# Kernel tuning notes

Measured on AMD Instinct MI355X. Metric: run time of the kernel, lower is better.

The kernel has to match this reference:

```python
import jax, jax.numpy as jnp
import numpy as np

D_MODEL = 1024
N_HEADS = 16
D_K = D_MODEL // N_HEADS
EPS = 1e-5


def setup_inputs() -> dict:
    key = jax.random.key(0)
    ks = jax.random.split(key, 10)
    s = 1.0 / np.sqrt(D_MODEL)
    x = jax.random.normal(ks[0], (4, 2048, D_MODEL), dtype=jnp.float32)
    def lin(k):
        kw, kb = jax.random.split(k)
        W = jax.random.uniform(kw, (D_MODEL, D_MODEL), jnp.float32, -s, s)
        b = jax.random.uniform(kb, (D_MODEL,), jnp.float32, -s, s)
        return W, b
    Wq, bq = lin(ks[1])
    Wk, bk = lin(ks[2])
    Wv, bv = lin(ks[3])
    Wo, bo = lin(ks[4])
    gamma = jnp.ones((D_MODEL,), jnp.float32)
    beta = jnp.zeros((D_MODEL,), jnp.float32)
    return {"x": x, "Wq": Wq, "bq": bq, "Wk": Wk, "bk": bk,
            "Wv": Wv, "bv": bv, "Wo": Wo, "bo": bo,
            "gamma": gamma, "beta": beta}


def reference(x, Wq, bq, Wk, bk, Wv, bv, Wo, bo, gamma, beta):
    b, n, _ = x.shape
    residual = x
    # projections (PyTorch Linear: x @ W.T + b; here W stored as [in,out]-equivalent via transpose-free matmul)
    q = x @ Wq.T + bq
    k = x @ Wk.T + bk
    v = x @ Wv.T + bv
    # b n (h d) -> b h n d
    q = q.reshape(b, n, N_HEADS, D_K).transpose(0, 2, 1, 3)
    k = k.reshape(b, n, N_HEADS, D_K).transpose(0, 2, 1, 3)
    v = v.reshape(b, n, N_HEADS, D_K).transpose(0, 2, 1, 3)
    scores = jnp.einsum('bhnd,bhmd->bhnm', q, k) / jnp.sqrt(jnp.float32(D_K))
    attn = jax.nn.softmax(scores, axis=-1)
    out = jnp.einsum('bhnm,bhmd->bhnd', attn, v)
    out = out.transpose(0, 2, 1, 3).reshape(b, n, D_MODEL)
    out = out @ Wo.T + bo
    h = residual + out
    mu = jnp.mean(h, axis=-1, keepdims=True)
    var = jnp.var(h, axis=-1, keepdims=True)
    out_ln = (h - mu) / jnp.sqrt(var + EPS) * gamma + beta
    return (out_ln, attn)
```

## Files before the change

### kernel.cpp

```cpp
#include <hip/hip_runtime.h>
#include <math.h>

#define D_MODEL 1024
#define N_HEADS 16
#define D_K     64
#define SEQ     2048
#define BATCH   4
#define EPS     1e-5f
#define NT      (SEQ / 64)

typedef __attribute__((ext_vector_type(8))) short bf16x8;
typedef __attribute__((ext_vector_type(4))) float f32x4;

__device__ __forceinline__ unsigned short f2bf(float f) {
    unsigned u = __float_as_uint(f);
    u += 0x7fff + ((u >> 16) & 1);
    return (unsigned short)(u >> 16);
}

#define GLDS16(g, l) __builtin_amdgcn_global_load_lds( \
    (const __attribute__((address_space(1))) void*)(g), \
    (__attribute__((address_space(3))) void*)(l), 16, 0, 0)

__global__ __launch_bounds__(256) void cvt_f32_bf16(
    const float* __restrict__ in, unsigned short* __restrict__ out, int n4)
{
    int i = blockIdx.x * 256 + threadIdx.x;
    if (i >= n4) return;
    float4 f = ((const float4*)in)[i];
    union { ushort4 u; uint2 v; } o;
    o.u.x = f2bf(f.x); o.u.y = f2bf(f.y); o.u.z = f2bf(f.z); o.u.w = f2bf(f.w);
    ((uint2*)out)[i] = o.v;
}

__global__ __launch_bounds__(256) void gemm_qkv(
    const unsigned short* __restrict__ A,
    const unsigned short* __restrict__ Bq, const unsigned short* __restrict__ Bk,
    const unsigned short* __restrict__ Bv,
    const float* __restrict__ biq, const float* __restrict__ bik,
    const float* __restrict__ biv,
    unsigned short* __restrict__ Oq, unsigned short* __restrict__ Ok,
    unsigned short* __restrict__ Ov)
{
    const int which = blockIdx.x >> 3;
    const unsigned short* B = which == 0 ? Bq : (which == 1 ? Bk : Bv);
    const float* bias        = which == 0 ? biq : (which == 1 ? bik : biv);
    unsigned short* O        = which == 0 ? Oq : (which == 1 ? Ok : Ov);
    const float scale        = which == 0 ? 0.125f : 1.0f;

    __shared__ unsigned short As[128 * 32];
    __shared__ unsigned short Bs[128 * 32];
    const int tid = threadIdx.x;
    const int w = tid >> 6, lane = tid & 63;
    const int l15 = lane & 15, lh = lane >> 4;
    const int wm = w >> 1, wn = w & 1;
    const int bm = blockIdx.y * 128, bn = (blockIdx.x & 7) * 128;
    const int K = D_MODEL, N = D_MODEL;

    const int srow = lane >> 2;
    const int skk  = (lane & 3) * 8;

    f32x4 acc[4][4] = {};

    for (int k0 = 0; k0 < K; k0 += 32) {
#pragma unroll
        for (int cc = 0; cc < 2; ++cc) {
            int chunk = w * 2 + cc;
            int row = chunk * 16 + srow;
            GLDS16(A + (size_t)(bm + row) * K + k0 + skk, As + chunk * 512);
            GLDS16(B + (size_t)(bn + row) * K + k0 + skk, Bs + chunk * 512);
        }
        __syncthreads();
        bf16x8 af[4], bfr[4];
#pragma unroll
        for (int mi = 0; mi < 4; ++mi)
            af[mi] = *(const bf16x8*)&As[(wm * 64 + mi * 16 + l15) * 32 + lh * 8];
#pragma unroll
        for (int nj = 0; nj < 4; ++nj)
            bfr[nj] = *(const bf16x8*)&Bs[(wn * 64 + nj * 16 + l15) * 32 + lh * 8];
#pragma unroll
        for (int mi = 0; mi < 4; ++mi)
#pragma unroll
            for (int nj = 0; nj < 4; ++nj)
                acc[mi][nj] = __builtin_amdgcn_mfma_f32_16x16x32_bf16(
                    af[mi], bfr[nj], acc[mi][nj], 0, 0, 0);
        __syncthreads();
    }

#pragma unroll
    for (int mi = 0; mi < 4; ++mi) {
#pragma unroll
        for (int nj = 0; nj < 4; ++nj) {
            int col = bn + wn * 64 + nj * 16 + l15;
            float bv = bias[col];
#pragma unroll
            for (int r = 0; r < 4; ++r) {
                int row = bm + wm * 64 + mi * 16 + lh * 4 + r;
                O[(size_t)row * N + col] = f2bf((acc[mi][nj][r] + bv) * scale);
            }
        }
    }
}

__global__ __launch_bounds__(256) void gemm_out(
    const unsigned short* __restrict__ A, const unsigned short* __restrict__ B,
    const float* __restrict__ bias, const float* __restrict__ res,
    float* __restrict__ C)
{
    __shared__ unsigned short As[128 * 32];
    __shared__ unsigned short Bs[128 * 32];
    const int tid = threadIdx.x;
    const int w = tid >> 6, lane = tid & 63;
    const int l15 = lane & 15, lh = lane >> 4;
    const int wm = w >> 1, wn = w & 1;
    const int bm = blockIdx.y * 128, bn = blockIdx.x * 128;
    const int K = D_MODEL, N = D_MODEL;

    const int srow = lane >> 2;
    const int skk  = (lane & 3) * 8;

    f32x4 acc[4][4] = {};

    for (int k0 = 0; k0 < K; k0 += 32) {
#pragma unroll
        for (int cc = 0; cc < 2; ++cc) {
            int chunk = w * 2 + cc;
            int row = chunk * 16 + srow;
            GLDS16(A + (size_t)(bm + row) * K + k0 + skk, As + chunk * 512);
            GLDS16(B + (size_t)(bn + row) * K + k0 + skk, Bs + chunk * 512);
        }
        __syncthreads();
        bf16x8 af[4], bfr[4];
#pragma unroll
        for (int mi = 0; mi < 4; ++mi)
            af[mi] = *(const bf16x8*)&As[(wm * 64 + mi * 16 + l15) * 32 + lh * 8];
#pragma unroll
        for (int nj = 0; nj < 4; ++nj)
            bfr[nj] = *(const bf16x8*)&Bs[(wn * 64 + nj * 16 + l15) * 32 + lh * 8];
#pragma unroll
        for (int mi = 0; mi < 4; ++mi)
#pragma unroll
            for (int nj = 0; nj < 4; ++nj)
                acc[mi][nj] = __builtin_amdgcn_mfma_f32_16x16x32_bf16(
                    af[mi], bfr[nj], acc[mi][nj], 0, 0, 0);
        __syncthreads();
    }

#pragma unroll
    for (int mi = 0; mi < 4; ++mi) {
#pragma unroll
        for (int nj = 0; nj < 4; ++nj) {
            int col = bn + wn * 64 + nj * 16 + l15;
            float bv = bias[col];
#pragma unroll
            for (int r = 0; r < 4; ++r) {
                int row = bm + wm * 64 + mi * 16 + lh * 4 + r;
                C[(size_t)row * N + col] = acc[mi][nj][r] + bv + res[(size_t)row * N + col];
            }
        }
    }
}

__global__ __launch_bounds__(256) void transpose_v(
    const unsigned short* __restrict__ v, unsigned short* __restrict__ vt)
{
    __shared__ unsigned short T[64][72];
    const int bh = blockIdx.y, b = bh >> 4, h = bh & 15;
    const int s0 = blockIdx.x * 64;
    const int tid = threadIdx.x;
#pragma unroll
    for (int i = 0; i < 2; ++i) {
        int idx = i * 256 + tid;
        int sr = idx >> 3, dc = idx & 7;
        uint4 t = *(const uint4*)(v + ((size_t)b * SEQ + s0 + sr) * D_MODEL + h * 64 + dc * 8);
        *(uint4*)&T[sr][dc * 8] = t;
    }
    __syncthreads();
#pragma unroll
    for (int i = 0; i < 2; ++i) {
        int idx = i * 256 + tid;
        int d = idx >> 3, sc = idx & 7;
        unsigned short tmp[8];
#pragma unroll
        for (int j = 0; j < 8; ++j) tmp[j] = T[sc * 8 + j][d];
        *(uint4*)(vt + ((size_t)bh * 64 + d) * SEQ + s0 + sc * 8) = *(uint4*)tmp;
    }
}

__device__ __forceinline__ void stage_tile64(
    const unsigned short* __restrict__ gbase, size_t grow_stride,
    unsigned short* lds, int w, int lane)
{
#pragma unroll
    for (int i = 0; i < 2; ++i) {
        int row = i * 32 + w * 8 + (lane >> 3);
        int c   = (lane & 7) ^ (row & 7);
        GLDS16(gbase + (size_t)row * grow_stride + c * 8,
               lds + (size_t)(i * 256 + w * 64) * 8);
    }
}

__global__ __launch_bounds__(256) void attn_pass0(
    const unsigned short* __restrict__ qb, const unsigned short* __restrict__ kb,
    float* __restrict__ invl)
{
    __shared__ unsigned short Ks[2][64 * 64];
    const int bh = blockIdx.x, b = bh >> 4, head = bh & 15;
    const int tid = threadIdx.x;
    const int w = tid >> 6, lane = tid & 63, l15 = lane & 15, lh = lane >> 4;
    const int bq = blockIdx.y * 128 + w * 32;
    const size_t rowbase = (size_t)b * SEQ;
    const unsigned short* Kh = kb + rowbase * D_MODEL + head * 64;

    bf16x8 aq[2][2];
#pragma unroll
    for (int qs = 0; qs < 2; ++qs)
#pragma unroll
        for (int kd = 0; kd < 2; ++kd)
            aq[qs][kd] = *(const bf16x8*)(qb + (rowbase + bq + qs * 16 + l15) * D_MODEL
                                          + head * 64 + kd * 32 + lh * 8);

    float rsum[2] = {0.f, 0.f};

    stage_tile64(Kh, D_MODEL, Ks[0], w, lane);
    __syncthreads();

    for (int kt = 0; kt < NT; ++kt) {
        const int cur = kt & 1;
        if (kt + 1 < NT)
            stage_tile64(Kh + (size_t)(kt + 1) * 64 * D_MODEL, D_MODEL, Ks[cur ^ 1], w, lane);

        const char* kbuf = (const char*)Ks[cur];
        f32x4 s[2][4] = {};
#pragma unroll
        for (int fj = 0; fj < 4; ++fj) {
            int key = fj * 16 + l15;
            bf16x8 kf0 = *(const bf16x8*)(kbuf + key * 128 + ((lh ^ (key & 7)) << 4));
            bf16x8 kf1 = *(const bf16x8*)(kbuf + key * 128 + (((4 + lh) ^ (key & 7)) << 4));
#pragma unroll
            for (int qs = 0; qs < 2; ++qs) {
                s[qs][fj] = __builtin_amdgcn_mfma_f32_16x16x32_bf16(kf0, aq[qs][0], s[qs][fj], 0, 0, 0);
                s[qs][fj] = __builtin_amdgcn_mfma_f32_16x16x32_bf16(kf1, aq[qs][1], s[qs][fj], 0, 0, 0);
            }
        }
#pragma unroll
        for (int qs = 0; qs < 2; ++qs)
#pragma unroll
            for (int fj = 0; fj < 4; ++fj)
                rsum[qs] += (__expf(s[qs][fj][0]) + __expf(s[qs][fj][1]))
                          + (__expf(s[qs][fj][2]) + __expf(s[qs][fj][3]));
        __syncthreads();
    }

#pragma unroll
    for (int qs = 0; qs < 2; ++qs) {
        float v = rsum[qs];
        v += __shfl_xor(v, 16, 64);
        v += __shfl_xor(v, 32, 64);
        if (lh == 0)
            invl[(size_t)bh * SEQ + bq + qs * 16 + l15] = 1.0f / v;
    }
}

__global__ __launch_bounds__(256) void attn_pass1(
    const unsigned short* __restrict__ qb, const unsigned short* __restrict__ kb,
    const unsigned short* __restrict__ vt, const float* __restrict__ invl,
    float* __restrict__ attnP, unsigned short* __restrict__ ctx)
{
    __shared__ unsigned short Ks[2][64 * 64];
    __shared__ unsigned short Vs[2][64 * 64];
    __shared__ unsigned short Ps[4][32 * 72];
    const int bh = blockIdx.x, b = bh >> 4, head = bh & 15;
    const int tid = threadIdx.x;
    const int w = tid >> 6, lane = tid & 63, l15 = lane & 15, lh = lane >> 4;
    const int bq = blockIdx.y * 128 + w * 32;
    const size_t rowbase = (size_t)b * SEQ;
    const unsigned short* Kh = kb + rowbase * D_MODEL + head * 64;
    const unsigned short* Vh = vt + (size_t)bh * 64 * SEQ;
    char* myPs = (char*)&Ps[w][0];

    bf16x8 aq[2][2];
    float invr[2];
    float* pdst[2];
#pragma unroll
    for (int qs = 0; qs < 2; ++qs) {
#pragma unroll
        for (int kd = 0; kd < 2; ++kd)
            aq[qs][kd] = *(const bf16x8*)(qb + (rowbase + bq + qs * 16 + l15) * D_MODEL
                                          + head * 64 + kd * 32 + lh * 8);
        invr[qs] = invl[(size_t)bh * SEQ + bq + qs * 16 + l15];
        pdst[qs] = attnP + ((size_t)bh * SEQ + bq + qs * 16 + l15) * SEQ + lh * 4;
    }

    f32x4 acc[2][4] = {};

    stage_tile64(Kh, D_MODEL, Ks[0], w, lane);
    stage_tile64(Vh, SEQ,     Vs[0], w, lane);
    __syncthreads();

    for (int kt = 0; kt < NT; ++kt) {
        const int cur = kt & 1;
        const int bk = kt * 64;
        if (kt + 1 < NT) {
            stage_tile64(Kh + (size_t)(bk + 64) * D_MODEL, D_MODEL, Ks[cur ^ 1], w, lane);
            stage_tile64(Vh + (size_t)(bk + 64),           SEQ,     Vs[cur ^ 1], w, lane);
        }

        const char* kbuf = (const char*)Ks[cur];
        f32x4 s[2][4] = {};
#pragma unroll
        for (int fj = 0; fj < 4; ++fj) {
            int key = fj * 16 + l15;
            bf16x8 kf0 = *(const bf16x8*)(kbuf + key * 128 + ((lh ^ (key & 7)) << 4));
            bf16x8 kf1 = *(const bf16x8*)(kbuf + key * 128 + (((4 + lh) ^ (key & 7)) << 4));
#pragma unroll
            for (int qs = 0; qs < 2; ++qs) {
                s[qs][fj] = __builtin_amdgcn_mfma_f32_16x16x32_bf16(kf0, aq[qs][0], s[qs][fj], 0, 0, 0);
                s[qs][fj] = __builtin_amdgcn_mfma_f32_16x16x32_bf16(kf1, aq[qs][1], s[qs][fj], 0, 0, 0);
            }
        }

#pragma unroll
        for (int qs = 0; qs < 2; ++qs) {
#pragma unroll
            for (int fj = 0; fj < 4; ++fj) {
                float p0 = __expf(s[qs][fj][0]) * invr[qs];
                float p1 = __expf(s[qs][fj][1]) * invr[qs];
                float p2 = __expf(s[qs][fj][2]) * invr[qs];
                float p3 = __expf(s[qs][fj][3]) * invr[qs];
                float4 st = {p0, p1, p2, p3};
                *(float4*)(pdst[qs] + bk + fj * 16) = st;
                uint2 pk;
                pk.x = ((unsigned)f2bf(p1) << 16) | f2bf(p0);
                pk.y = ((unsigned)f2bf(p3) << 16) | f2bf(p2);
                *(uint2*)(myPs + (qs * 16 + l15) * 144 + fj * 32 + lh * 8) = pk;
            }
        }

        const char* vbuf = (const char*)Vs[cur];
        bf16x8 pb[2][2];
#pragma unroll
        for (int qs = 0; qs < 2; ++qs)
#pragma unroll
            for (int ks = 0; ks < 2; ++ks)
                pb[qs][ks] = *(const bf16x8*)(myPs + (qs * 16 + l15) * 144 + ks * 64 + lh * 16);
#pragma unroll
        for (int db = 0; db < 4; ++db) {
            int d = db * 16 + l15;
            bf16x8 va0 = *(const bf16x8*)(vbuf + d * 128 + ((lh ^ (d & 7)) << 4));
            bf16x8 va1 = *(const bf16x8*)(vbuf + d * 128 + (((4 + lh) ^ (d & 7)) << 4));
#pragma unroll
            for (int qs = 0; qs < 2; ++qs) {
                acc[qs][db] = __builtin_amdgcn_mfma_f32_16x16x32_bf16(va0, pb[qs][0], acc[qs][db], 0, 0, 0);
                acc[qs][db] = __builtin_amdgcn_mfma_f32_16x16x32_bf16(va1, pb[qs][1], acc[qs][db], 0, 0, 0);
            }
        }
        __syncthreads();
    }

#pragma unroll
    for (int qs = 0; qs < 2; ++qs)
#pragma unroll
        for (int db = 0; db < 4; ++db) {
            union { ushort4 u; uint2 v; } o;
            o.u.x = f2bf(acc[qs][db][0]); o.u.y = f2bf(acc[qs][db][1]);
            o.u.z = f2bf(acc[qs][db][2]); o.u.w = f2bf(acc[qs][db][3]);
            *(uint2*)&ctx[(rowbase + bq + qs * 16 + l15) * D_MODEL + head * 64 + db * 16 + lh * 4] = o.v;
        }
}

__global__ __launch_bounds__(256) void layernorm_rows(
    const float* __restrict__ h, const float* __restrict__ gamma,
    const float* __restrict__ beta, float* __restrict__ out)
{
    const size_t row = blockIdx.x;
    const float* hr = h + row * D_MODEL;
    const int tid = threadIdx.x;

    float v[4];
    float s = 0.f;
#pragma unroll
    for (int i = 0; i < 4; ++i) { v[i] = hr[tid + i * 256]; s += v[i]; }
    __shared__ float red[256];
    red[tid] = s;
    __syncthreads();
    for (int st = 128; st > 0; st >>= 1) {
        if (tid < st) red[tid] += red[tid + st];
        __syncthreads();
    }
    float mean = red[0] * (1.0f / D_MODEL);
    __syncthreads();

    float vs = 0.f;
#pragma unroll
    for (int i = 0; i < 4; ++i) { float d = v[i] - mean; vs += d * d; }
    red[tid] = vs;
    __syncthreads();
    for (int st = 128; st > 0; st >>= 1) {
        if (tid < st) red[tid] += red[tid + st];
        __syncthreads();
    }
    float inv = rsqrtf(red[0] * (1.0f / D_MODEL) + EPS);

#pragma unroll
    for (int i = 0; i < 4; ++i) {
        int c = tid + i * 256;
        out[row * D_MODEL + c] = (v[i] - mean) * inv * gamma[c] + beta[c];
    }
}

extern "C" void kernel_launch(void* const* d_in, const int* in_sizes, int n_in,
                              void* d_out, int out_size, void* d_ws, size_t ws_size,
                              hipStream_t stream)
{
    const float* x     = (const float*)d_in[0];
    const float* Wq    = (const float*)d_in[1];
    const float* bq_   = (const float*)d_in[2];
    const float* Wk    = (const float*)d_in[3];
    const float* bk_   = (const float*)d_in[4];
    const float* Wv    = (const float*)d_in[5];
    const float* bv_   = (const float*)d_in[6];
    const float* Wo    = (const float*)d_in[7];
    const float* bo_   = (const float*)d_in[8];
    const float* gamma = (const float*)d_in[9];
    const float* beta  = (const float*)d_in[10];

    const size_t NX = (size_t)BATCH * SEQ * D_MODEL;
    const size_t NW = (size_t)D_MODEL * D_MODEL;

    float* out_ln = (float*)d_out;
    float* attnP  = out_ln + NX;

    unsigned short* x_bf   = (unsigned short*)d_ws;
    unsigned short* wq_bf  = x_bf + NX;
    unsigned short* wk_bf  = wq_bf + NW;
    unsigned short* wv_bf  = wk_bf + NW;
    unsigned short* wo_bf  = wv_bf + NW;
    unsigned short* q_bf   = wo_bf + NW;
    unsigned short* k_bf   = q_bf + NX;
    unsigned short* v_bf   = k_bf + NX;
    unsigned short* ctx_bf = v_bf + NX;
    float* invl = (float*)(ctx_bf + NX);
    unsigned short* vt_bf = x_bf;
    float* hbuf = (float*)q_bf;

    const int M = BATCH * SEQ;

    cvt_f32_bf16<<<(int)(NX / 4 / 256), 256, 0, stream>>>(x, x_bf, (int)(NX / 4));
    cvt_f32_bf16<<<(int)(NW / 4 / 256), 256, 0, stream>>>(Wq, wq_bf, (int)(NW / 4));
    cvt_f32_bf16<<<(int)(NW / 4 / 256), 256, 0, stream>>>(Wk, wk_bf, (int)(NW / 4));
    cvt_f32_bf16<<<(int)(NW / 4 / 256), 256, 0, stream>>>(Wv, wv_bf, (int)(NW / 4));
    cvt_f32_bf16<<<(int)(NW / 4 / 256), 256, 0, stream>>>(Wo, wo_bf, (int)(NW / 4));

    gemm_qkv<<<dim3(24, M / 128), 256, 0, stream>>>(
        x_bf, wq_bf, wk_bf, wv_bf, bq_, bk_, bv_, q_bf, k_bf, v_bf);

    transpose_v<<<dim3(SEQ / 64, BATCH * N_HEADS), 256, 0, stream>>>(v_bf, vt_bf);

    attn_pass0<<<dim3(BATCH * N_HEADS, SEQ / 128), 256, 0, stream>>>(q_bf, k_bf, invl);

    attn_pass1<<<dim3(BATCH * N_HEADS, SEQ / 128), 256, 0, stream>>>(
        q_bf, k_bf, vt_bf, invl, attnP, ctx_bf);

    gemm_out<<<dim3(D_MODEL / 128, M / 128), 256, 0, stream>>>(
        ctx_bf, wo_bf, bo_, x, hbuf);

    layernorm_rows<<<M, 256, 0, stream>>>(hbuf, gamma, beta, out_ln);
}
```

Baseline: 533.6 us.

## Fuse conversions, write V transposed from QKV GEMM, nontemporal attn stores

Merges the five f32-to-bf16 conversion launches into a single kernel and drops the separate V transpose kernel. The QKV GEMM epilogue now writes V directly in head-major transposed layout, packing four consecutive sequence rows per store. The attention-probability output is written with nontemporal stores so the large attn matrix does not pollute cache. The transposed V epilogue uses 8-byte scattered stores with a large stride, which may coalesce less well than the row-major writes it replaces.

New measurement: 584.3 us. +9.5%, slower.

```diff
diff --git a/kernel.cpp b/kernel.cpp
--- a/kernel.cpp
+++ b/kernel.cpp
@@ -22,15 +22,32 @@
     (const __attribute__((address_space(1))) void*)(g), \
     (__attribute__((address_space(3))) void*)(l), 16, 0, 0)
 
-__global__ __launch_bounds__(256) void cvt_f32_bf16(
-    const float* __restrict__ in, unsigned short* __restrict__ out, int n4)
-{
-    int i = blockIdx.x * 256 + threadIdx.x;
-    if (i >= n4) return;
-    float4 f = ((const float4*)in)[i];
+__global__ __launch_bounds__(256) void cvt_all(
+    const float* __restrict__ x,
+    const float* __restrict__ Wq, const float* __restrict__ Wk,
+    const float* __restrict__ Wv, const float* __restrict__ Wo,
+    unsigned short* __restrict__ xb,
+    unsigned short* __restrict__ wqb, unsigned short* __restrict__ wkb,
+    unsigned short* __restrict__ wvb, unsigned short* __restrict__ wob)
+{
+    size_t i4 = (size_t)blockIdx.x * 256 + threadIdx.x;
+    const float* src; unsigned short* dst; size_t off;
+    if (i4 < 2097152) { src = x; dst = xb; off = i4; }
+    else {
+        size_t j = i4 - 2097152;
+        int wsel = (int)(j >> 18);
+        off = j & 262143;
+        switch (wsel) {
+            case 0:  src = Wq; dst = wqb; break;
+            case 1:  src = Wk; dst = wkb; break;
+            case 2:  src = Wv; dst = wvb; break;
+            default: src = Wo; dst = wob; break;
+        }
+    }
+    float4 f = ((const float4*)src)[off];
     union { ushort4 u; uint2 v; } o;
     o.u.x = f2bf(f.x); o.u.y = f2bf(f.y); o.u.z = f2bf(f.z); o.u.w = f2bf(f.w);
-    ((uint2*)out)[i] = o.v;
+    ((uint2*)dst)[off] = o.v;
 }
 
 __global__ __launch_bounds__(256) void gemm_qkv(
@@ -40,12 +57,11 @@
     const float* __restrict__ biq, const float* __restrict__ bik,
     const float* __restrict__ biv,
     unsigned short* __restrict__ Oq, unsigned short* __restrict__ Ok,
-    unsigned short* __restrict__ Ov)
+    unsigned short* __restrict__ Vt)
 {
     const int which = blockIdx.x >> 3;
     const unsigned short* B = which == 0 ? Bq : (which == 1 ? Bk : Bv);
     const float* bias        = which == 0 ? biq : (which == 1 ? bik : biv);
-    unsigned short* O        = which == 0 ? Oq : (which == 1 ? Ok : Ov);
     const float scale        = which == 0 ? 0.125f : 1.0f;
 
     __shared__ unsigned short As[128 * 32];
@@ -87,16 +103,37 @@
         __syncthreads();
     }
 
-#pragma unroll
-    for (int mi = 0; mi < 4; ++mi) {
-#pragma unroll
-        for (int nj = 0; nj < 4; ++nj) {
-            int col = bn + wn * 64 + nj * 16 + l15;
-            float bv = bias[col];
-#pragma unroll
-            for (int r = 0; r < 4; ++r) {
-                int row = bm + wm * 64 + mi * 16 + lh * 4 + r;
-                O[(size_t)row * N + col] = f2bf((acc[mi][nj][r] + bv) * scale);
+    if (which == 2) {
+#pragma unroll
+        for (int mi = 0; mi < 4; ++mi) {
+#pragma unroll
+            for (int nj = 0; nj < 4; ++nj) {
+                int col = bn + wn * 64 + nj * 16 + l15;
+                int head = col >> 6, d = col & 63;
+                float bv = bias[col];
+                int row = bm + wm * 64 + mi * 16 + lh * 4;
+                int b = row >> 11, s = row & 2047;
+                union { ushort4 u; uint2 v; } o;
+                o.u.x = f2bf(acc[mi][nj][0] + bv);
+                o.u.y = f2bf(acc[mi][nj][1] + bv);
+                o.u.z = f2bf(acc[mi][nj][2] + bv);
+                o.u.w = f2bf(acc[mi][nj][3] + bv);
+                *(uint2*)&Vt[(((size_t)b * 16 + head) * 64 + d) * SEQ + s] = o.v;
+            }
+        }
+    } else {
+        unsigned short* O = which == 0 ? Oq : Ok;
+#pragma unroll
+        for (int mi = 0; mi < 4; ++mi) {
+#pragma unroll
+            for (int nj = 0; nj < 4; ++nj) {
+                int col = bn + wn * 64 + nj * 16 + l15;
+                float bv = bias[col];
+#pragma unroll
+                for (int r = 0; r < 4; ++r) {
+                    int row = bm + wm * 64 + mi * 16 + lh * 4 + r;
+                    O[(size_t)row * N + col] = f2bf((acc[mi][nj][r] + bv) * scale);
+                }
             }
         }
     }
@@ -158,32 +195,6 @@
                 C[(size_t)row * N + col] = acc[mi][nj][r] + bv + res[(size_t)row * N + col];
             }
         }
-    }
-}
-
-__global__ __launch_bounds__(256) void transpose_v(
-    const unsigned short* __restrict__ v, unsigned short* __restrict__ vt)
-{
-    __shared__ unsigned short T[64][72];
-    const int bh = blockIdx.y, b = bh >> 4, h = bh & 15;
-    const int s0 = blockIdx.x * 64;
-    const int tid = threadIdx.x;
-#pragma unroll
-    for (int i = 0; i < 2; ++i) {
-        int idx = i * 256 + tid;
-        int sr = idx >> 3, dc = idx & 7;
-        uint4 t = *(const uint4*)(v + ((size_t)b * SEQ + s0 + sr) * D_MODEL + h * 64 + dc * 8);
-        *(uint4*)&T[sr][dc * 8] = t;
-    }
-    __syncthreads();
-#pragma unroll
-    for (int i = 0; i < 2; ++i) {
-        int idx = i * 256 + tid;
-        int d = idx >> 3, sc = idx & 7;
-        unsigned short tmp[8];
-#pragma unroll
-        for (int j = 0; j < 8; ++j) tmp[j] = T[sc * 8 + j][d];
-        *(uint4*)(vt + ((size_t)bh * 64 + d) * SEQ + s0 + sc * 8) = *(uint4*)tmp;
     }
 }
 
@@ -328,8 +339,8 @@
                 float p1 = __expf(s[qs][fj][1]) * invr[qs];
                 float p2 = __expf(s[qs][fj][2]) * invr[qs];
                 float p3 = __expf(s[qs][fj][3]) * invr[qs];
-                float4 st = {p0, p1, p2, p3};
-                *(float4*)(pdst[qs] + bk + fj * 16) = st;
+                f32x4 st = {p0, p1, p2, p3};
+                __builtin_nontemporal_store(st, (f32x4*)(pdst[qs] + bk + fj * 16));
                 uint2 pk;
                 pk.x = ((unsigned)f2bf(p1) << 16) | f2bf(p0);
                 pk.y = ((unsigned)f2bf(p3) << 16) | f2bf(p2);
@@ -438,24 +449,18 @@
     unsigned short* wo_bf  = wv_bf + NW;
     unsigned short* q_bf   = wo_bf + NW;
     unsigned short* k_bf   = q_bf + NX;
-    unsigned short* v_bf   = k_bf + NX;
-    unsigned short* ctx_bf = v_bf + NX;
+    unsigned short* vt_bf  = k_bf + NX;
+    unsigned short* ctx_bf = vt_bf + NX;
     float* invl = (float*)(ctx_bf + NX);
-    unsigned short* vt_bf = x_bf;
     float* hbuf = (float*)q_bf;
 
     const int M = BATCH * SEQ;
 
-    cvt_f32_bf16<<<(int)(NX / 4 / 256), 256, 0, stream>>>(x, x_bf, (int)(NX / 4));
-    cvt_f32_bf16<<<(int)(NW / 4 / 256), 256, 0, stream>>>(Wq, wq_bf, (int)(NW / 4));
-    cvt_f32_bf16<<<(int)(NW / 4 / 256), 256, 0, stream>>>(Wk, wk_bf, (int)(NW / 4));
-    cvt_f32_bf16<<<(int)(NW / 4 / 256), 256, 0, stream>>>(Wv, wv_bf, (int)(NW / 4));
-    cvt_f32_bf16<<<(int)(NW / 4 / 256), 256, 0, stream>>>(Wo, wo_bf, (int)(NW / 4));
+    cvt_all<<<12288, 256, 0, stream>>>(x, Wq, Wk, Wv, Wo,
+                                       x_bf, wq_bf, wk_bf, wv_bf, wo_bf);
 
     gemm_qkv<<<dim3(24, M / 128), 256, 0, stream>>>(
-        x_bf, wq_bf, wk_bf, wv_bf, bq_, bk_, bv_, q_bf, k_bf, v_bf);
-
-    transpose_v<<<dim3(SEQ / 64, BATCH * N_HEADS), 256, 0, stream>>>(v_bf, vt_bf);
+        x_bf, wq_bf, wk_bf, wv_bf, bq_, bk_, bv_, q_bf, k_bf, vt_bf);
 
     attn_pass0<<<dim3(BATCH * N_HEADS, SEQ / 128), 256, 0, stream>>>(q_bf, k_bf, invl);
 
```
